# Optimization experiments

Hardware: AMD Instinct MI355X
Metric: run time of the kernel (lower is better)

The kernel has to match this reference:

```python
import jax, jax.numpy as jnp
import numpy as np

NUM_CLASSES = 20
IGNORE_THRESH = 0.5
COORD_SCALE = 1.0
NOOBJ_SCALE = 1.0
OBJ_SCALE = 1.0
CLASS_SCALE = 1.0


def pairwise_iou_xywh(a, b):
    # a: (..., N, 4), b: (..., M, 4), boxes in (cx, cy, w, h) -> IoU (..., N, M)
    ae = a[..., :, None, :]
    be = b[..., None, :, :]
    tl = jnp.maximum(ae[..., :2] - ae[..., 2:] * 0.5, be[..., :2] - be[..., 2:] * 0.5)
    br = jnp.minimum(ae[..., :2] + ae[..., 2:] * 0.5, be[..., :2] + be[..., 2:] * 0.5)
    wh = jnp.maximum(br - tl, 0.0)
    inter = wh[..., 0] * wh[..., 1]
    area_a = ae[..., 2] * ae[..., 3]
    area_b = be[..., 2] * be[..., 3]
    return inter / (area_a + area_b - inter)


def build_targets(outputs, targets, anchors):
    # outputs detached in the torch code -> constants w.r.t. the network output
    o = jax.lax.stop_gradient(outputs)
    B, C, H, W = o.shape
    A = anchors.shape[0]
    HW = H * W
    ch = 5 + NUM_CLASSES
    o5 = o.reshape(B, A, ch, H, W).transpose(0, 1, 3, 4, 2)  # (B, A, H, W, ch)

    x_shift = jnp.arange(W, dtype=o.dtype)            # (W,)
    y_shift = jnp.arange(H, dtype=o.dtype)[:, None]   # (H, 1)
    px = jax.nn.sigmoid(o5[..., 0]) + x_shift
    py = jax.nn.sigmoid(o5[..., 1]) + y_shift
    pw = jnp.exp(o5[..., 2]) * anchors[:, 0][:, None, None]
    ph = jnp.exp(o5[..., 3]) * anchors[:, 1][:, None, None]
    pred = jnp.stack([px, py, pw, ph], -1).transpose(0, 2, 3, 1, 4).reshape(B, HW, A, 4)

    # per-cell anchor boxes, corner-anchored (x_cell, y_cell, aw, ah)
    xs = jnp.broadcast_to(x_shift, (H, W))
    ys = jnp.broadcast_to(jnp.arange(H, dtype=o.dtype)[:, None], (H, W))
    anc = jnp.stack([
        jnp.broadcast_to(xs[:, :, None], (H, W, A)),
        jnp.broadcast_to(ys[:, :, None], (H, W, A)),
        jnp.broadcast_to(anchors[:, 0], (H, W, A)),
        jnp.broadcast_to(anchors[:, 1], (H, W, A))], -1).reshape(HW, A, 4)
    anc_c = anc.at[..., :2].add(0.5)  # center form

    M = targets.shape[1]
    num_obj = jnp.sum(jnp.sum(targets, -1) > 0, axis=1)          # (B,)
    valid = jnp.arange(M)[None, :] < num_obj[:, None]            # (B, M)
    scale = jnp.array([W, H, W, H], o.dtype)
    gt = targets[..., 1:] * scale                                # (B, M, 4) in grid units
    gcls = targets[..., 0]

    # IoU between every pred box and every gt box
    ious = pairwise_iou_xywh(pred.reshape(B, HW * A, 4), gt).reshape(B, HW, A, M)
    ious = jnp.where(valid[:, None, None, :], ious, 0.0)
    max_iou = jnp.max(ious, axis=-1)                             # (B, HW, A)
    has_pos = jnp.any((max_iou > IGNORE_THRESH).reshape(B, -1), axis=1)
    iou_mask = jnp.where(has_pos[:, None, None] & (max_iou >= IGNORE_THRESH), 0.0, 1.0)
    iou_mask = jnp.where((num_obj == 0)[:, None, None], 0.0, iou_mask)

    # anchor/gt overlaps for responsibility assignment
    overlaps = pairwise_iou_xywh(anc_c.reshape(HW * A, 4)[None], gt).reshape(B, HW, A, M)

    cell = (jnp.floor(gt[..., 1]) * W + jnp.floor(gt[..., 0])).astype(jnp.int32)
    cell = jnp.clip(cell, 0, HW - 1)                             # (B, M)
    ov = jnp.take_along_axis(overlaps.transpose(0, 3, 1, 2), cell[:, :, None, None], axis=2)[:, :, 0, :]  # (B, M, A)
    anchor_idx = jnp.argmax(ov, axis=-1)                         # (B, M)
    bidx = jnp.arange(B)[:, None]

    anc_sel = anc[cell, anchor_idx]                              # (B, M, 4)
    delta = jnp.stack([gt[..., 0] - anc_sel[..., 0],
                       gt[..., 1] - anc_sel[..., 1],
                       gt[..., 2] / anc_sel[..., 2],
                       gt[..., 3] / anc_sel[..., 3]], -1)        # (B, M, 4)
    pred_sel = pred[bidx, cell, anchor_idx]                      # (B, M, 4)
    bscale = 2.0 - (pred_sel[..., 2] / W) * (pred_sel[..., 3] / H)
    miou_sel = max_iou[bidx, cell, anchor_idx]                   # (B, M)

    iou_target = jnp.zeros((B, HW, A), o.dtype)
    box_target = jnp.zeros((B, HW, A, 4), o.dtype)
    box_mask = jnp.zeros((B, HW, A), o.dtype)
    box_scale = jnp.zeros((B, HW, A), o.dtype)
    class_target = jnp.zeros((B, HW, A), jnp.int32)
    class_mask = jnp.zeros((B, HW, A), o.dtype)
    b_ar = jnp.arange(B)

    def step(carry, inp):
        it, im, bt, bm, bs, ct, cm = carry
        c, a, v, d, sc, mi, cl = inp
        c_safe = jnp.where(v, c, HW)  # out-of-range -> dropped for padded objects
        it = it.at[b_ar, c_safe, a].set(mi, mode='drop')
        im = im.at[b_ar, c_safe, a].set(2.0, mode='drop')
        bt = bt.at[b_ar, c_safe, a].set(d, mode='drop')
        bm = bm.at[b_ar, c_safe, a].set(1.0, mode='drop')
        bs = bs.at[b_ar, c_safe, a].set(sc, mode='drop')
        ct = ct.at[b_ar, c_safe, a].set(cl.astype(jnp.int32), mode='drop')
        cm = cm.at[b_ar, c_safe, a].set(1.0, mode='drop')
        return (it, im, bt, bm, bs, ct, cm), None

    xs_scan = (cell.T, anchor_idx.T, valid.T, delta.transpose(1, 0, 2),
               bscale.T, miou_sel.T, gcls.T)
    carry, _ = jax.lax.scan(step, (iou_target, iou_mask, box_target, box_mask,
                                   box_scale, class_target, class_mask), xs_scan)
    it, im, bt, bm, bs, ct, cm = carry
    return (it.reshape(-1), im.reshape(-1), bt.reshape(-1, 4), bm.reshape(-1),
            bs.reshape(-1, 1), ct.reshape(-1), cm.reshape(-1))


def yolov2_loss(outputs, targets, anchors):
    it, im, bt, bm, bs, ct, cm = build_targets(outputs, targets, anchors)
    B, C, H, W = outputs.shape
    A = anchors.shape[0]
    ch = 5 + NUM_CLASSES
    o = outputs.reshape(B, A, ch, H, W).transpose(0, 3, 4, 1, 2).reshape(B, H * W * A, ch)
    pred_deltas = jnp.concatenate([jax.nn.sigmoid(o[..., :2]), jnp.exp(o[..., 2:4])], -1).reshape(-1, 4)
    pred_confs = jax.nn.sigmoid(o[..., 4]).reshape(-1)
    pred_probs = o[..., 5:].reshape(-1, NUM_CLASSES)

    s = jnp.sqrt(bs)  # (N, 1); bs is a stop-gradient constant
    box_loss = jnp.sum(bm[:, None] * ((pred_deltas - bt) * s) ** 2)
    obj_iou_loss = jnp.sum(jnp.where(im == 2.0, (pred_confs - it) ** 2, 0.0))
    noobj_iou_loss = jnp.sum(jnp.where(im == 1.0, (pred_confs - it) ** 2, 0.0))
    logp = jax.nn.log_softmax(pred_probs, axis=-1)
    ce = -jnp.take_along_axis(logp, ct[:, None], axis=1)[:, 0]
    class_loss = jnp.sum(cm * ce)
    loss = (COORD_SCALE * box_loss + OBJ_SCALE * obj_iou_loss +
            NOOBJ_SCALE * noobj_iou_loss + CLASS_SCALE * class_loss)
    return loss / B


def setup_inputs() -> dict:
    key = jax.random.key(0)
    k1, k2, k3, k4, k5 = jax.random.split(key, 5)
    B, H, W, A, M = 128, 26, 26, 5, 64
    outputs = jax.random.normal(k1, (B, A * (5 + NUM_CLASSES), H, W), jnp.float32) * 0.5
    cls = jax.random.randint(k2, (B, M, 1), 0, NUM_CLASSES).astype(jnp.float32)
    xy = jax.random.uniform(k3, (B, M, 2), minval=0.05, maxval=0.95)
    wh = jax.random.uniform(k4, (B, M, 2), minval=0.05, maxval=0.5)
    targets = jnp.concatenate([cls, xy, wh], -1)  # (cls, xc, yc, w, h) normalized
    num_obj = jax.random.randint(k5, (B,), 1, M + 1)
    valid = (jnp.arange(M)[None, :] < num_obj[:, None]).astype(jnp.float32)
    targets = targets * valid[:, :, None]  # zero-pad invalid rows (matches gt_num_objs logic)
    anchors = jnp.array([[1.3221, 1.73145], [3.19275, 4.00944], [5.05587, 8.09892],
                         [9.47112, 4.84053], [11.2364, 10.0071]], jnp.float32)
    return {"outputs": outputs, "targets": targets, "anchors": anchors}


def reference(outputs, targets, anchors):
    return yolov2_loss(outputs, targets, anchors)
```

## Files before the change

kernel.cpp:

```cpp
#include <hip/hip_runtime.h>
#include <math.h>

#define NCLS 20
#define B_N 128
#define A_N 5
#define H_N 26
#define W_N 26
#define HW_N (H_N * W_N)
#define M_N 64
#define CH_N (5 + NCLS)
#define HALF_LOC (HW_N / 2)
#define HALF_T (HALF_LOC / 2)
#define BLK_T 192
#define WIN_BLKS B_N
#define NOOBJ_BLKS (B_N * A_N * 2)
#define PARTS_PER_B (A_N * 2)

__device__ __forceinline__ float fastrcp(float x) { return __builtin_amdgcn_rcpf(x); }
__device__ __forceinline__ float sigmoidf_(float x) { return fastrcp(1.0f + __expf(-x)); }

__global__ __launch_bounds__(BLK_T) void main_kernel(
    const float* __restrict__ outputs, const float* __restrict__ targets,
    const float* __restrict__ anchors,
    float* __restrict__ A_part, float* __restrict__ H_part,
    int* __restrict__ any_part,
    float* __restrict__ Gb, float* __restrict__ Asub, float* __restrict__ Hsub,
    int* __restrict__ nobjArr) {
    int blk = blockIdx.x;
    bool winnerBlk = (blk < WIN_BLKS);
    int nb = blk - WIN_BLKS;
    int plane = nb >> 1;
    int half = nb & 1;
    int b = winnerBlk ? blk : (plane / A_N);
    int a = winnerBlk ? 0 : (plane % A_N);
    int tid = threadIdx.x;

    __shared__ float4 sg4[M_N];
    __shared__ float sgx[M_N], sgy[M_N], sgw[M_N], sgh[M_N], sc[M_N];
    __shared__ int skey[M_N];
    __shared__ int snobj;
    __shared__ float rA[3], rH[3];
    __shared__ int rAny[3];

    if (tid < M_N) {
        const float* trow = targets + ((size_t)b * M_N + tid) * 5;
        float tc = trow[0], tx = trow[1], ty = trow[2], tw = trow[3], th = trow[4];
        bool valid = (tc + tx + ty + tw + th) > 0.0f;
        unsigned long long mask = __ballot(valid);
        if (tid == 0) snobj = __popcll(mask);
        float gx = tx * (float)W_N, gy = ty * (float)H_N;
        float gw = tw * (float)W_N, gh = th * (float)H_N;
        sg4[tid] = make_float4(gx - gw * 0.5f, gy - gh * 0.5f,
                               gx + gw * 0.5f, gy + gh * 0.5f);
        sgx[tid] = gx; sgy[tid] = gy; sgw[tid] = gw; sgh[tid] = gh; sc[tid] = tc;
    }
    __syncthreads();
    int nobj = snobj;

    if (winnerBlk) {
        float G = 0.0f, c2A = 0.0f, c2H = 0.0f;
        if (tid < M_N) {
            int m = tid;
            bool valid = (m < nobj);
            float gx = sgx[m], gy = sgy[m];
            float4 g4 = sg4[m];
            float ga = sgw[m] * sgh[m];
            int cell = (int)floorf(gy) * W_N + (int)floorf(gx);
            cell = min(max(cell, 0), HW_N - 1);
            int ccx = cell % W_N, ccy = cell / W_N;
            float best = -1.0f;
            int ai = 0; float aw = 1.0f, ah = 1.0f;
            #pragma unroll
            for (int aa = 0; aa < A_N; ++aa) {
                float anw = anchors[2 * aa], anh = anchors[2 * aa + 1];
                float atlx = (float)ccx + 0.5f - anw * 0.5f;
                float atly = (float)ccy + 0.5f - anh * 0.5f;
                float ix = fminf(atlx + anw, g4.z) - fmaxf(atlx, g4.x);
                float iy = fminf(atly + anh, g4.w) - fmaxf(atly, g4.y);
                float inter = fmaxf(ix, 0.0f) * fmaxf(iy, 0.0f);
                float ov = inter * fastrcp(anw * anh + ga - inter);
                if (ov > best) { best = ov; ai = aa; aw = anw; ah = anh; }
            }
            skey[m] = valid ? (cell * A_N + ai) : -1;
            __builtin_amdgcn_s_waitcnt(0);

            bool winner = valid;
            if (valid) {
                int mykey = skey[m];
                for (int mm = m + 1; mm < M_N; ++mm)
                    if (skey[mm] == mykey) winner = false;
            }

            if (winner) {
                size_t obase = ((size_t)b * (A_N * CH_N) + (size_t)ai * CH_N) * HW_N + cell;
                float o0 = outputs[obase + 0 * HW_N];
                float o1 = outputs[obase + 1 * HW_N];
                float o2 = outputs[obase + 2 * HW_N];
                float o3 = outputs[obase + 3 * HW_N];
                float o4 = outputs[obase + 4 * HW_N];
                float sx = sigmoidf_(o0), sy = sigmoidf_(o1);
                float ew = __expf(o2), eh = __expf(o3);
                float conf = sigmoidf_(o4);
                float px = sx + (float)ccx, py = sy + (float)ccy;
                float pw = ew * aw, ph = eh * ah;
                float ptlx = px - pw * 0.5f, ptly = py - ph * 0.5f;
                float pbrx = px + pw * 0.5f, pbry = py + ph * 0.5f;
                float pa = pw * ph;

                float mi = 0.0f, maxdW = -1e30f;
                for (int mm = 0; mm < nobj; ++mm) {
                    float4 g = sg4[mm];
                    float gaM = (g.z - g.x) * (g.w - g.y);
                    float ix = fminf(pbrx, g.z) - fmaxf(ptlx, g.x);
                    float iy = fminf(pbry, g.w) - fmaxf(ptly, g.y);
                    float inter = fmaxf(ix, 0.0f) * fmaxf(iy, 0.0f);
                    mi = fmaxf(mi, inter * fastrcp(pa + gaM - inter));
                    maxdW = fmaxf(maxdW, fmaf(3.0f, inter, -(pa + gaM)));
                }

                float dcf = conf - mi;
                G = dcf * dcf;
                float bs = 2.0f - (pw / (float)W_N) * (ph / (float)H_N);
                float e0 = sx - (gx - (float)ccx);
                float e1 = sy - (gy - (float)ccy);
                float e2 = ew - sgw[m] / aw;
                float e3 = eh - sgh[m] / ah;
                G += bs * (e0 * e0 + e1 * e1 + e2 * e2 + e3 * e3);

                int cls = (int)sc[m];
                float mx = -1e30f, tv = 0.0f, logits[NCLS];
                #pragma unroll
                for (int c = 0; c < NCLS; ++c) {
                    logits[c] = outputs[obase + (size_t)(5 + c) * HW_N];
                    mx = fmaxf(mx, logits[c]);
                }
                float se = 0.0f;
                #pragma unroll
                for (int c = 0; c < NCLS; ++c) {
                    se += __expf(logits[c] - mx);
                    if (c == cls) tv = logits[c];
                }
                G += (mx + __logf(se)) - tv;

                c2A = conf * conf;
                c2H = (maxdW >= 0.0f) ? c2A : 0.0f;
            }
            #pragma unroll
            for (int off = 32; off > 0; off >>= 1) {
                G   += __shfl_down(G, off);
                c2A += __shfl_down(c2A, off);
                c2H += __shfl_down(c2H, off);
            }
            if (tid == 0) {
                Gb[b] = G; Asub[b] = c2A; Hsub[b] = c2H; nobjArr[b] = nobj;
            }
        }
    } else {
        float locA = 0.0f, locH = 0.0f;
        bool any = false;
        if (tid < HALF_T) {
            int hw0 = half * HALF_LOC + tid * 2;
            size_t obase = ((size_t)b * (A_N * CH_N) + (size_t)a * CH_N) * HW_N;
            float2 O0 = *(const float2*)(outputs + obase + 0 * HW_N + hw0);
            float2 O1 = *(const float2*)(outputs + obase + 1 * HW_N + hw0);
            float2 O2 = *(const float2*)(outputs + obase + 2 * HW_N + hw0);
            float2 O3 = *(const float2*)(outputs + obase + 3 * HW_N + hw0);
            float2 O4 = *(const float2*)(outputs + obase + 4 * HW_N + hw0);
            float aw = anchors[2 * a], ah = anchors[2 * a + 1];

            int wy = hw0 / W_N;
            int wx = hw0 - wy * W_N;

            float sx0 = sigmoidf_(O0.x), sx1 = sigmoidf_(O0.y);
            float sy0 = sigmoidf_(O1.x), sy1 = sigmoidf_(O1.y);
            float pw0 = __expf(O2.x) * aw, pw1 = __expf(O2.y) * aw;
            float ph0 = __expf(O3.x) * ah, ph1 = __expf(O3.y) * ah;
            float px0 = sx0 + (float)wx, px1 = sx1 + (float)(wx + 1);
            float py0 = sy0 + (float)wy, py1 = sy1 + (float)wy;

            float ptlx0 = px0 - pw0 * 0.5f, ptly0 = py0 - ph0 * 0.5f;
            float pbrx0 = px0 + pw0 * 0.5f, pbry0 = py0 + ph0 * 0.5f;
            float ptlx1 = px1 - pw1 * 0.5f, ptly1 = py1 - ph1 * 0.5f;
            float pbrx1 = px1 + pw1 * 0.5f, pbry1 = py1 + ph1 * 0.5f;
            float pa0 = pw0 * ph0, pa1 = pw1 * ph1;

            float maxd0 = -1e30f, maxd1 = -1e30f;
            #pragma unroll 2
            for (int m = 0; m < nobj; ++m) {
                float4 g = sg4[m];
                float ga = (g.z - g.x) * (g.w - g.y);
                float t0 = pa0 + ga, t1 = pa1 + ga;
                float ix0 = fminf(pbrx0, g.z) - fmaxf(ptlx0, g.x);
                float iy0 = fminf(pbry0, g.w) - fmaxf(ptly0, g.y);
                float in0 = fmaxf(ix0, 0.0f) * fmaxf(iy0, 0.0f);
                maxd0 = fmaxf(maxd0, fmaf(3.0f, in0, -t0));
                float ix1 = fminf(pbrx1, g.z) - fmaxf(ptlx1, g.x);
                float iy1 = fminf(pbry1, g.w) - fmaxf(ptly1, g.y);
                float in1 = fmaxf(ix1, 0.0f) * fmaxf(iy1, 0.0f);
                maxd1 = fmaxf(maxd1, fmaf(3.0f, in1, -t1));
            }
            float conf0 = sigmoidf_(O4.x), conf1 = sigmoidf_(O4.y);
            float c20 = conf0 * conf0, c21 = conf1 * conf1;
            locA = c20 + c21;
            locH = (maxd0 >= 0.0f ? c20 : 0.0f) + (maxd1 >= 0.0f ? c21 : 0.0f);
            any = (maxd0 > 0.0f) || (maxd1 > 0.0f);
        }

        int wany = __any(any) ? 1 : 0;
        #pragma unroll
        for (int off = 32; off > 0; off >>= 1) {
            locA += __shfl_down(locA, off);
            locH += __shfl_down(locH, off);
        }
        int wave = tid >> 6, lane = tid & 63;
        if (lane == 0) { rA[wave] = locA; rH[wave] = locH; rAny[wave] = wany; }
        __syncthreads();
        if (tid == 0) {
            A_part[nb] = rA[0] + rA[1] + rA[2];
            H_part[nb] = rH[0] + rH[1] + rH[2];
            any_part[nb] = rAny[0] | rAny[1] | rAny[2];
        }
    }
}

__global__ __launch_bounds__(128) void finish_kernel(
    const float* __restrict__ A_part, const float* __restrict__ H_part,
    const int* __restrict__ any_part,
    const float* __restrict__ Gb, const float* __restrict__ Asub,
    const float* __restrict__ Hsub, const int* __restrict__ nobjArr,
    float* __restrict__ out) {
    int t = threadIdx.x;
    float A = -Asub[t], Hs = -Hsub[t];
    int any = 0;
    #pragma unroll
    for (int j = 0; j < PARTS_PER_B; ++j) {
        A += A_part[t * PARTS_PER_B + j];
        Hs += H_part[t * PARTS_PER_B + j];
        any |= any_part[t * PARTS_PER_B + j];
    }
    float noobj = (nobjArr[t] > 0) ? (A - (any ? Hs : 0.0f)) : 0.0f;
    float v = Gb[t] + noobj;
    #pragma unroll
    for (int off = 32; off > 0; off >>= 1) v += __shfl_down(v, off);
    __shared__ float r[2];
    if ((t & 63) == 0) r[t >> 6] = v;
    __syncthreads();
    if (t == 0) out[0] = (r[0] + r[1]) / (float)B_N;
}

extern "C" void kernel_launch(void* const* d_in, const int* in_sizes, int n_in,
                              void* d_out, int out_size, void* d_ws, size_t ws_size,
                              hipStream_t stream) {
    const float* outputs = (const float*)d_in[0];
    const float* targets = (const float*)d_in[1];
    const float* anchors = (const float*)d_in[2];
    float* out = (float*)d_out;

    char* ws = (char*)d_ws;
    size_t off = 0;
    float* A_part = (float*)(ws + off); off += 4 * (size_t)NOOBJ_BLKS;
    float* H_part = (float*)(ws + off); off += 4 * (size_t)NOOBJ_BLKS;
    int* any_part = (int*)(ws + off);   off += 4 * (size_t)NOOBJ_BLKS;
    float* Gb = (float*)(ws + off);     off += 4 * B_N;
    float* Asub = (float*)(ws + off);   off += 4 * B_N;
    float* Hsub = (float*)(ws + off);   off += 4 * B_N;
    int* nobjArr = (int*)(ws + off);    off += 4 * B_N;

    main_kernel<<<WIN_BLKS + NOOBJ_BLKS, BLK_T, 0, stream>>>(
        outputs, targets, anchors,
        A_part, H_part, any_part, Gb, Asub, Hsub, nobjArr);

    finish_kernel<<<1, 128, 0, stream>>>(A_part, H_part, any_part,
                                         Gb, Asub, Hsub, nobjArr, out);
}
```

Baseline: 19.33 us.

## Remove block barriers via per-wave GT copies, atomic winner dedup, and per-wave partials

Each wave now loads and stages its own copy of the ground-truth boxes in shared memory, so no __syncthreads is needed. Invalid boxes get sentinel coordinates, which lets the IoU loops run to a multiple of eight and unroll. Winner deduplication changes from an O(M) key scan to a shared-memory atomicMax owner table. Per-wave partial sums are written straight to global slots, and the finish kernel reduces three times as many slots. Output loads are hoisted ahead of the target staging to overlap latency. The barrier-free owner-table handshake relies on single-wave execution in winner blocks.

Result: slower. 20.60 us (+6.6%).

```diff
diff --git a/kernel.cpp b/kernel.cpp
--- a/kernel.cpp
+++ b/kernel.cpp
@@ -12,9 +12,13 @@
 #define HALF_LOC (HW_N / 2)
 #define HALF_T (HALF_LOC / 2)
 #define BLK_T 192
+#define WAVES_PB 3
 #define WIN_BLKS B_N
 #define NOOBJ_BLKS (B_N * A_N * 2)
-#define PARTS_PER_B (A_N * 2)
+#define SLOTS (NOOBJ_BLKS * WAVES_PB)
+#define SLOTS_PER_B (A_N * 2 * WAVES_PB)
+
+#define SENT 1.0e18f
 
 __device__ __forceinline__ float fastrcp(float x) { return __builtin_amdgcn_rcpf(x); }
 __device__ __forceinline__ float sigmoidf_(float x) { return fastrcp(1.0f + __expf(-x)); }
@@ -28,148 +32,149 @@
     int* __restrict__ nobjArr) {
     int blk = blockIdx.x;
     bool winnerBlk = (blk < WIN_BLKS);
+    int tid = threadIdx.x;
+    if (winnerBlk && tid >= M_N) return;
+    int w = tid >> 6, lane = tid & 63;
     int nb = blk - WIN_BLKS;
-    int plane = nb >> 1;
-    int half = nb & 1;
+    int plane = nb >> 1, half = nb & 1;
     int b = winnerBlk ? blk : (plane / A_N);
     int a = winnerBlk ? 0 : (plane % A_N);
-    int tid = threadIdx.x;
-
-    __shared__ float4 sg4[M_N];
-    __shared__ float sgx[M_N], sgy[M_N], sgw[M_N], sgh[M_N], sc[M_N];
-    __shared__ int skey[M_N];
-    __shared__ int snobj;
-    __shared__ float rA[3], rH[3];
-    __shared__ int rAny[3];
-
-    if (tid < M_N) {
-        const float* trow = targets + ((size_t)b * M_N + tid) * 5;
-        float tc = trow[0], tx = trow[1], ty = trow[2], tw = trow[3], th = trow[4];
-        bool valid = (tc + tx + ty + tw + th) > 0.0f;
-        unsigned long long mask = __ballot(valid);
-        if (tid == 0) snobj = __popcll(mask);
-        float gx = tx * (float)W_N, gy = ty * (float)H_N;
-        float gw = tw * (float)W_N, gh = th * (float)H_N;
-        sg4[tid] = make_float4(gx - gw * 0.5f, gy - gh * 0.5f,
-                               gx + gw * 0.5f, gy + gh * 0.5f);
-        sgx[tid] = gx; sgy[tid] = gy; sgw[tid] = gw; sgh[tid] = gh; sc[tid] = tc;
+
+    __shared__ float4 sg4[WAVES_PB * M_N];
+    __shared__ int owner[HW_N * A_N];
+
+    const float* trow = targets + ((size_t)b * M_N + lane) * 5;
+    float tc = trow[0], tx = trow[1], ty = trow[2], tw = trow[3], th = trow[4];
+
+    float2 O0, O1, O2, O3, O4;
+    int hw0 = 0;
+    bool act = false;
+    if (!winnerBlk) {
+        act = (tid < HALF_T);
+        if (act) {
+            hw0 = half * HALF_LOC + tid * 2;
+            const float* op = outputs +
+                ((size_t)b * (A_N * CH_N) + (size_t)a * CH_N) * HW_N + hw0;
+            O0 = *(const float2*)(op + 0 * HW_N);
+            O1 = *(const float2*)(op + 1 * HW_N);
+            O2 = *(const float2*)(op + 2 * HW_N);
+            O3 = *(const float2*)(op + 3 * HW_N);
+            O4 = *(const float2*)(op + 4 * HW_N);
+        }
     }
-    __syncthreads();
-    int nobj = snobj;
+
+    bool valid = (tc + tx + ty + tw + th) > 0.0f;
+    unsigned long long mask = __ballot(valid);
+    int nobj = __popcll(mask);
+    int nobj8 = (nobj + 7) & ~7;
+    float gx = tx * (float)W_N, gy = ty * (float)H_N;
+    float gw = tw * (float)W_N, gh = th * (float)H_N;
+    float4 g4 = valid ? make_float4(gx - gw * 0.5f, gy - gh * 0.5f,
+                                    gx + gw * 0.5f, gy + gh * 0.5f)
+                      : make_float4(SENT, SENT, SENT, SENT);
+    float4* myg = sg4 + w * M_N;
+    myg[lane] = g4;
+    __threadfence_block();
 
     if (winnerBlk) {
         float G = 0.0f, c2A = 0.0f, c2H = 0.0f;
-        if (tid < M_N) {
-            int m = tid;
-            bool valid = (m < nobj);
-            float gx = sgx[m], gy = sgy[m];
-            float4 g4 = sg4[m];
-            float ga = sgw[m] * sgh[m];
-            int cell = (int)floorf(gy) * W_N + (int)floorf(gx);
-            cell = min(max(cell, 0), HW_N - 1);
-            int ccx = cell % W_N, ccy = cell / W_N;
-            float best = -1.0f;
-            int ai = 0; float aw = 1.0f, ah = 1.0f;
+        int m = lane;
+        int cell = (int)floorf(gy) * W_N + (int)floorf(gx);
+        cell = min(max(cell, 0), HW_N - 1);
+        int ccx = cell % W_N, ccy = cell / W_N;
+        float best = -1.0f;
+        int ai = 0; float aw = 1.0f, ah = 1.0f;
+        float ga = gw * gh;
+        #pragma unroll
+        for (int aa = 0; aa < A_N; ++aa) {
+            float anw = anchors[2 * aa], anh = anchors[2 * aa + 1];
+            float atlx = (float)ccx + 0.5f - anw * 0.5f;
+            float atly = (float)ccy + 0.5f - anh * 0.5f;
+            float ix = fminf(atlx + anw, g4.z) - fmaxf(atlx, g4.x);
+            float iy = fminf(atly + anh, g4.w) - fmaxf(atly, g4.y);
+            float inter = fmaxf(ix, 0.0f) * fmaxf(iy, 0.0f);
+            float ov = inter * fastrcp(anw * anh + ga - inter);
+            if (ov > best) { best = ov; ai = aa; aw = anw; ah = anh; }
+        }
+        int mykey = cell * A_N + ai;
+
+        if (valid) owner[mykey] = 0;
+        __threadfence_block();
+        if (valid) atomicMax(&owner[mykey], m);
+        __threadfence_block();
+        bool winner = valid && (owner[mykey] == m);
+
+        if (winner) {
+            size_t obase = ((size_t)b * (A_N * CH_N) + (size_t)ai * CH_N) * HW_N + cell;
+            float o0 = outputs[obase + 0 * HW_N];
+            float o1 = outputs[obase + 1 * HW_N];
+            float o2 = outputs[obase + 2 * HW_N];
+            float o3 = outputs[obase + 3 * HW_N];
+            float o4 = outputs[obase + 4 * HW_N];
+            float sx = sigmoidf_(o0), sy = sigmoidf_(o1);
+            float ew = __expf(o2), eh = __expf(o3);
+            float conf = sigmoidf_(o4);
+            float px = sx + (float)ccx, py = sy + (float)ccy;
+            float pw = ew * aw, ph = eh * ah;
+            float ptlx = px - pw * 0.5f, ptly = py - ph * 0.5f;
+            float pbrx = px + pw * 0.5f, pbry = py + ph * 0.5f;
+            float pa = pw * ph;
+
+            float mi = 0.0f, maxdW = -1e30f;
+            #pragma unroll 4
+            for (int mm = 0; mm < nobj8; ++mm) {
+                float4 g = myg[mm];
+                float gaM = (g.z - g.x) * (g.w - g.y);
+                float ix = fminf(pbrx, g.z) - fmaxf(ptlx, g.x);
+                float iy = fminf(pbry, g.w) - fmaxf(ptly, g.y);
+                float inter = fmaxf(ix, 0.0f) * fmaxf(iy, 0.0f);
+                mi = fmaxf(mi, inter * fastrcp(pa + gaM - inter));
+                maxdW = fmaxf(maxdW, fmaf(3.0f, inter, -(pa + gaM)));
+            }
+
+            float dcf = conf - mi;
+            G = dcf * dcf;
+            float bs = 2.0f - (pw / (float)W_N) * (ph / (float)H_N);
+            float e0 = sx - (gx - (float)ccx);
+            float e1 = sy - (gy - (float)ccy);
+            float e2 = ew - gw / aw;
+            float e3 = eh - gh / ah;
+            G += bs * (e0 * e0 + e1 * e1 + e2 * e2 + e3 * e3);
+
+            int cls = (int)tc;
+            float mx = -1e30f, tv = 0.0f, logits[NCLS];
             #pragma unroll
-            for (int aa = 0; aa < A_N; ++aa) {
-                float anw = anchors[2 * aa], anh = anchors[2 * aa + 1];
-                float atlx = (float)ccx + 0.5f - anw * 0.5f;
-                float atly = (float)ccy + 0.5f - anh * 0.5f;
-                float ix = fminf(atlx + anw, g4.z) - fmaxf(atlx, g4.x);
-                float iy = fminf(atly + anh, g4.w) - fmaxf(atly, g4.y);
-                float inter = fmaxf(ix, 0.0f) * fmaxf(iy, 0.0f);
-                float ov = inter * fastrcp(anw * anh + ga - inter);
-                if (ov > best) { best = ov; ai = aa; aw = anw; ah = anh; }
-            }
-            skey[m] = valid ? (cell * A_N + ai) : -1;
-            __builtin_amdgcn_s_waitcnt(0);
-
-            bool winner = valid;
-            if (valid) {
-                int mykey = skey[m];
-                for (int mm = m + 1; mm < M_N; ++mm)
-                    if (skey[mm] == mykey) winner = false;
-            }
-
-            if (winner) {
-                size_t obase = ((size_t)b * (A_N * CH_N) + (size_t)ai * CH_N) * HW_N + cell;
-                float o0 = outputs[obase + 0 * HW_N];
-                float o1 = outputs[obase + 1 * HW_N];
-                float o2 = outputs[obase + 2 * HW_N];
-                float o3 = outputs[obase + 3 * HW_N];
-                float o4 = outputs[obase + 4 * HW_N];
-                float sx = sigmoidf_(o0), sy = sigmoidf_(o1);
-                float ew = __expf(o2), eh = __expf(o3);
-                float conf = sigmoidf_(o4);
-                float px = sx + (float)ccx, py = sy + (float)ccy;
-                float pw = ew * aw, ph = eh * ah;
-                float ptlx = px - pw * 0.5f, ptly = py - ph * 0.5f;
-                float pbrx = px + pw * 0.5f, pbry = py + ph * 0.5f;
-                float pa = pw * ph;
-
-                float mi = 0.0f, maxdW = -1e30f;
-                for (int mm = 0; mm < nobj; ++mm) {
-                    float4 g = sg4[mm];
-                    float gaM = (g.z - g.x) * (g.w - g.y);
-                    float ix = fminf(pbrx, g.z) - fmaxf(ptlx, g.x);
-                    float iy = fminf(pbry, g.w) - fmaxf(ptly, g.y);
-                    float inter = fmaxf(ix, 0.0f) * fmaxf(iy, 0.0f);
-                    mi = fmaxf(mi, inter * fastrcp(pa + gaM - inter));
-                    maxdW = fmaxf(maxdW, fmaf(3.0f, inter, -(pa + gaM)));
-                }
-
-                float dcf = conf - mi;
-                G = dcf * dcf;
-                float bs = 2.0f - (pw / (float)W_N) * (ph / (float)H_N);
-                float e0 = sx - (gx - (float)ccx);
-                float e1 = sy - (gy - (float)ccy);
-                float e2 = ew - sgw[m] / aw;
-                float e3 = eh - sgh[m] / ah;
-                G += bs * (e0 * e0 + e1 * e1 + e2 * e2 + e3 * e3);
-
-                int cls = (int)sc[m];
-                float mx = -1e30f, tv = 0.0f, logits[NCLS];
-                #pragma unroll
-                for (int c = 0; c < NCLS; ++c) {
-                    logits[c] = outputs[obase + (size_t)(5 + c) * HW_N];
-                    mx = fmaxf(mx, logits[c]);
-                }
-                float se = 0.0f;
-                #pragma unroll
-                for (int c = 0; c < NCLS; ++c) {
-                    se += __expf(logits[c] - mx);
-                    if (c == cls) tv = logits[c];
-                }
-                G += (mx + __logf(se)) - tv;
-
-                c2A = conf * conf;
-                c2H = (maxdW >= 0.0f) ? c2A : 0.0f;
-            }
+            for (int c = 0; c < NCLS; ++c) {
+                logits[c] = outputs[obase + (size_t)(5 + c) * HW_N];
+                mx = fmaxf(mx, logits[c]);
+            }
+            float se = 0.0f;
             #pragma unroll
-            for (int off = 32; off > 0; off >>= 1) {
-                G   += __shfl_down(G, off);
-                c2A += __shfl_down(c2A, off);
-                c2H += __shfl_down(c2H, off);
-            }
-            if (tid == 0) {
-                Gb[b] = G; Asub[b] = c2A; Hsub[b] = c2H; nobjArr[b] = nobj;
-            }
+            for (int c = 0; c < NCLS; ++c) {
+                se += __expf(logits[c] - mx);
+                if (c == cls) tv = logits[c];
+            }
+            G += (mx + __logf(se)) - tv;
+
+            c2A = conf * conf;
+            c2H = (maxdW >= 0.0f) ? c2A : 0.0f;
+        }
+        #pragma unroll
+        for (int off = 32; off > 0; off >>= 1) {
+            G   += __shfl_down(G, off);
+            c2A += __shfl_down(c2A, off);
+            c2H += __shfl_down(c2H, off);
+        }
+        if (lane == 0) {
+            Gb[b] = G; Asub[b] = c2A; Hsub[b] = c2H; nobjArr[b] = nobj;
         }
     } else {
         float locA = 0.0f, locH = 0.0f;
         bool any = false;
-        if (tid < HALF_T) {
-            int hw0 = half * HALF_LOC + tid * 2;
-            size_t obase = ((size_t)b * (A_N * CH_N) + (size_t)a * CH_N) * HW_N;
-            float2 O0 = *(const float2*)(outputs + obase + 0 * HW_N + hw0);
-            float2 O1 = *(const float2*)(outputs + obase + 1 * HW_N + hw0);
-            float2 O2 = *(const float2*)(outputs + obase + 2 * HW_N + hw0);
-            float2 O3 = *(const float2*)(outputs + obase + 3 * HW_N + hw0);
-            float2 O4 = *(const float2*)(outputs + obase + 4 * HW_N + hw0);
-            float aw = anchors[2 * a], ah = anchors[2 * a + 1];
-
+        if (act) {
             int wy = hw0 / W_N;
             int wx = hw0 - wy * W_N;
+            float aw = anchors[2 * a], ah = anchors[2 * a + 1];
 
             float sx0 = sigmoidf_(O0.x), sx1 = sigmoidf_(O0.y);
             float sy0 = sigmoidf_(O1.x), sy1 = sigmoidf_(O1.y);
@@ -185,19 +190,20 @@
             float pa0 = pw0 * ph0, pa1 = pw1 * ph1;
 
             float maxd0 = -1e30f, maxd1 = -1e30f;
-            #pragma unroll 2
-            for (int m = 0; m < nobj; ++m) {
-                float4 g = sg4[m];
-                float ga = (g.z - g.x) * (g.w - g.y);
-                float t0 = pa0 + ga, t1 = pa1 + ga;
-                float ix0 = fminf(pbrx0, g.z) - fmaxf(ptlx0, g.x);
-                float iy0 = fminf(pbry0, g.w) - fmaxf(ptly0, g.y);
-                float in0 = fmaxf(ix0, 0.0f) * fmaxf(iy0, 0.0f);
-                maxd0 = fmaxf(maxd0, fmaf(3.0f, in0, -t0));
-                float ix1 = fminf(pbrx1, g.z) - fmaxf(ptlx1, g.x);
-                float iy1 = fminf(pbry1, g.w) - fmaxf(ptly1, g.y);
-                float in1 = fmaxf(ix1, 0.0f) * fmaxf(iy1, 0.0f);
-                maxd1 = fmaxf(maxd1, fmaf(3.0f, in1, -t1));
+            for (int m = 0; m < nobj8; m += 8) {
+                #pragma unroll
+                for (int k = 0; k < 8; ++k) {
+                    float4 g = myg[m + k];
+                    float ga = (g.z - g.x) * (g.w - g.y);
+                    float ix0 = fminf(pbrx0, g.z) - fmaxf(ptlx0, g.x);
+                    float iy0 = fminf(pbry0, g.w) - fmaxf(ptly0, g.y);
+                    float in0 = fmaxf(ix0, 0.0f) * fmaxf(iy0, 0.0f);
+                    maxd0 = fmaxf(maxd0, fmaf(3.0f, in0, -(pa0 + ga)));
+                    float ix1 = fminf(pbrx1, g.z) - fmaxf(ptlx1, g.x);
+                    float iy1 = fminf(pbry1, g.w) - fmaxf(ptly1, g.y);
+                    float in1 = fmaxf(ix1, 0.0f) * fmaxf(iy1, 0.0f);
+                    maxd1 = fmaxf(maxd1, fmaf(3.0f, in1, -(pa1 + ga)));
+                }
             }
             float conf0 = sigmoidf_(O4.x), conf1 = sigmoidf_(O4.y);
             float c20 = conf0 * conf0, c21 = conf1 * conf1;
@@ -212,13 +218,11 @@
             locA += __shfl_down(locA, off);
             locH += __shfl_down(locH, off);
         }
-        int wave = tid >> 6, lane = tid & 63;
-        if (lane == 0) { rA[wave] = locA; rH[wave] = locH; rAny[wave] = wany; }
-        __syncthreads();
-        if (tid == 0) {
-            A_part[nb] = rA[0] + rA[1] + rA[2];
-            H_part[nb] = rH[0] + rH[1] + rH[2];
-            any_part[nb] = rAny[0] | rAny[1] | rAny[2];
+        if (lane == 0) {
+            int slot = nb * WAVES_PB + w;
+            A_part[slot] = locA;
+            H_part[slot] = locH;
+            any_part[slot] = wany;
         }
     }
 }
@@ -233,10 +237,10 @@
     float A = -Asub[t], Hs = -Hsub[t];
     int any = 0;
     #pragma unroll
-    for (int j = 0; j < PARTS_PER_B; ++j) {
-        A += A_part[t * PARTS_PER_B + j];
-        Hs += H_part[t * PARTS_PER_B + j];
-        any |= any_part[t * PARTS_PER_B + j];
+    for (int j = 0; j < SLOTS_PER_B; ++j) {
+        A += A_part[t * SLOTS_PER_B + j];
+        Hs += H_part[t * SLOTS_PER_B + j];
+        any |= any_part[t * SLOTS_PER_B + j];
     }
     float noobj = (nobjArr[t] > 0) ? (A - (any ? Hs : 0.0f)) : 0.0f;
     float v = Gb[t] + noobj;
@@ -258,9 +262,9 @@
 
     char* ws = (char*)d_ws;
     size_t off = 0;
-    float* A_part = (float*)(ws + off); off += 4 * (size_t)NOOBJ_BLKS;
-    float* H_part = (float*)(ws + off); off += 4 * (size_t)NOOBJ_BLKS;
-    int* any_part = (int*)(ws + off);   off += 4 * (size_t)NOOBJ_BLKS;
+    float* A_part = (float*)(ws + off); off += 4 * (size_t)SLOTS;
+    float* H_part = (float*)(ws + off); off += 4 * (size_t)SLOTS;
+    int* any_part = (int*)(ws + off);   off += 4 * (size_t)SLOTS;
     float* Gb = (float*)(ws + off);     off += 4 * B_N;
     float* Asub = (float*)(ws + off);   off += 4 * B_N;
     float* Hsub = (float*)(ws + off);   off += 4 * B_N;
```
